# Optimization experiments

Measured on AMD Instinct MI355X. Metric: run time of the kernel, lower is better.

## Reference

```python
import jax, jax.numpy as jnp
import numpy as np

B, S, D = 4, 2048, 1024


def setup_inputs() -> dict:
    key = jax.random.key(0)
    k1, k2, k3, k4 = jax.random.split(key, 4)
    scale = 1.0 / np.sqrt(D)
    return {
        "X_emb": jax.random.normal(k1, (B, S, D), dtype=jnp.float32),
        "W_q": jax.random.normal(k2, (D, D), dtype=jnp.float32) * scale,
        "W_k": jax.random.normal(k3, (D, D), dtype=jnp.float32) * scale,
        "W_v": jax.random.normal(k4, (D, D), dtype=jnp.float32) * scale,
    }


def reference(X_emb, W_q, W_k, W_v):
    # nn.Linear(bias=False): x @ W.T
    Xq = jnp.einsum('bsd,ed->bse', X_emb, W_q)
    Xk = jnp.einsum('bsd,ed->bse', X_emb, W_k)
    Xv = jnp.einsum('bsd,ed->bse', X_emb, W_v)
    S_len = X_emb.shape[-2]
    # scores [B, S, S]; causal mask (strict upper triangle -> -inf)
    att = jnp.einsum('bqe,bke->bqk', Xq, Xk)
    causal = jnp.tril(jnp.ones((S_len, S_len), dtype=bool))
    att = jnp.where(causal, att, -jnp.inf)
    # note: original masks before scaling; -inf / sqrt(d) is still -inf
    att = att / jnp.sqrt(jnp.asarray(Xk.shape[-1], att.dtype))
    w = jax.nn.softmax(att, axis=-1)
    return jnp.einsum('bqk,bke->bqe', w, Xv)
```

## Files before the change

### kernel.cpp

```cpp
#include <hip/hip_runtime.h>
#include <stdint.h>
#include <math.h>

typedef __attribute__((ext_vector_type(8))) __bf16 bf16x8;
typedef __attribute__((ext_vector_type(4))) float f32x4;

__device__ __forceinline__ unsigned short f2bf(float f) {
    unsigned u = __float_as_uint(f);
    u += 0x7FFF + ((u >> 16) & 1);
    return (unsigned short)(u >> 16);
}
__device__ __forceinline__ float bf2f(unsigned short u) {
    return __uint_as_float((unsigned)u << 16);
}

__global__ __launch_bounds__(256)
void convt_k(const float* __restrict__ X, const float* __restrict__ Wq,
             const float* __restrict__ Wk, const float* __restrict__ Wv,
             unsigned short* __restrict__ Xb, unsigned short* __restrict__ WqT,
             unsigned short* __restrict__ WkT, unsigned short* __restrict__ Wvb,
             float* __restrict__ outz) {
    const int S = 2048, D = 1024;
    const int z = blockIdx.z;
    const int t = threadIdx.x;
    if (z == 7) {
        int gid = (blockIdx.y * 16 + blockIdx.x) * 256 + t;
        int stride = 512 * 256;
        float4 zz = (float4){0.f, 0.f, 0.f, 0.f};
        for (int i = gid; i < 4 * S * D / 4; i += stride)
            reinterpret_cast<float4*>(outz)[i] = zz;
        return;
    }
    const float* src;
    unsigned short* dstP = nullptr;
    unsigned short* dstT = nullptr;
    int rows;
    if (z < 4)      { src = X + (size_t)z * S * D; dstP = Xb + (size_t)z * S * D; rows = S; }
    else if (z == 4){ src = Wq; dstT = WqT; rows = D; }
    else if (z == 5){ src = Wk; dstT = WkT; rows = D; }
    else            { src = Wv; dstP = Wvb; rows = D; }
    const int r0 = blockIdx.y * 64, c0 = blockIdx.x * 64;
    if (r0 >= rows) return;

    __shared__ float tile[64][65];
    const int tr = t >> 4;
    const int tc4 = t & 15;
#pragma unroll
    for (int p = 0; p < 4; ++p) {
        int r = p * 16 + tr;
        float4 v = *reinterpret_cast<const float4*>(&src[(size_t)(r0 + r) * 1024 + c0 + tc4 * 4]);
        if (dstP) {
            ushort4 o; o.x = f2bf(v.x); o.y = f2bf(v.y); o.z = f2bf(v.z); o.w = f2bf(v.w);
            *reinterpret_cast<ushort4*>(&dstP[(size_t)(r0 + r) * 1024 + c0 + tc4 * 4]) = o;
        }
        if (dstT) {
            tile[r][tc4 * 4 + 0] = v.x; tile[r][tc4 * 4 + 1] = v.y;
            tile[r][tc4 * 4 + 2] = v.z; tile[r][tc4 * 4 + 3] = v.w;
        }
    }
    if (!dstT) return;
    __syncthreads();
#pragma unroll
    for (int p = 0; p < 4; ++p) {
        int c = p * 16 + tr;
        ushort4 o;
        o.x = f2bf(tile[tc4 * 4 + 0][c]);
        o.y = f2bf(tile[tc4 * 4 + 1][c]);
        o.z = f2bf(tile[tc4 * 4 + 2][c]);
        o.w = f2bf(tile[tc4 * 4 + 3][c]);
        *reinterpret_cast<ushort4*>(&dstT[(size_t)(c0 + c) * 1024 + r0 + tc4 * 4]) = o;
    }
}

__global__ __launch_bounds__(256)
void reduce4_k(const float* __restrict__ p, unsigned short* __restrict__ o, int n4) {
    const int slab = 1024 * 1024 / 4;
    int i = blockIdx.x * blockDim.x + threadIdx.x;
    int stride = gridDim.x * blockDim.x;
    for (; i < n4; i += stride) {
        float4 a = reinterpret_cast<const float4*>(p)[i];
        float4 b = reinterpret_cast<const float4*>(p)[i + slab];
        float4 c = reinterpret_cast<const float4*>(p)[i + 2 * slab];
        float4 d = reinterpret_cast<const float4*>(p)[i + 3 * slab];
        ushort4 u;
        u.x = f2bf(a.x + b.x + c.x + d.x);
        u.y = f2bf(a.y + b.y + c.y + d.y);
        u.z = f2bf(a.z + b.z + c.z + d.z);
        u.w = f2bf(a.w + b.w + c.w + d.w);
        reinterpret_cast<ushort4*>(o)[i] = u;
    }
}

__device__ __forceinline__ void gload16(const unsigned short* g, unsigned short* l) {
    __builtin_amdgcn_global_load_lds(
        (const __attribute__((address_space(1))) unsigned int*)g,
        (__attribute__((address_space(3))) unsigned int*)l, 16, 0, 0);
}

template <typename CT, bool ATOMIC>
__device__ __forceinline__ void core_tile(
    const unsigned short* __restrict__ A, const unsigned short* __restrict__ B,
    CT* __restrict__ C, int lda, int ldb, int ldc,
    int m0, int n0, int kst, int nk, float scale, bool first,
    unsigned short* AsB, unsigned short* BsB)
{
    const int t    = threadIdx.x;
    const int lane = t & 63;
    const int wid  = t >> 6;
    const int wm   = wid >> 1, wn = wid & 1;
    const int rsel = lane & 15;
    const int gsel = lane >> 4;
    const int srow = t >> 3;
    const int swz  = ((t & 7) ^ (srow & 7)) * 8;

    f32x4 acc[4][4];
#pragma unroll
    for (int m = 0; m < 4; ++m)
#pragma unroll
        for (int n = 0; n < 4; ++n) acc[m][n] = (f32x4){0.f, 0.f, 0.f, 0.f};

    const unsigned short* gpA[4];
    const unsigned short* gpB[4];
#pragma unroll
    for (int i = 0; i < 4; ++i) {
        gpA[i] = A + (long long)(m0 + srow + 32 * i) * lda + kst * 64 + swz;
        gpB[i] = B + (long long)(n0 + srow + 32 * i) * ldb + kst * 64 + swz;
    }

    auto stage = [&](int buf) {
#pragma unroll
        for (int i = 0; i < 4; ++i)
            gload16(gpA[i], &AsB[buf * 8192 + i * 2048 + t * 8]);
#pragma unroll
        for (int i = 0; i < 4; ++i)
            gload16(gpB[i], &BsB[buf * 8192 + i * 2048 + t * 8]);
#pragma unroll
        for (int i = 0; i < 4; ++i) { gpA[i] += 64; gpB[i] += 64; }
    };

    if (!first) {
        __builtin_amdgcn_s_barrier();
        __builtin_amdgcn_sched_barrier(0);
    }
    stage(0);

    for (int kt = 0; kt < nk; ++kt) {
        const int c = kt & 1;
        __builtin_amdgcn_s_barrier();
        __builtin_amdgcn_sched_barrier(0);
        if (kt + 1 < nk) {
            stage(c ^ 1);
            asm volatile("s_waitcnt vmcnt(8)" ::: "memory");
        } else {
            asm volatile("s_waitcnt vmcnt(0)" ::: "memory");
        }
        __builtin_amdgcn_s_barrier();
        __builtin_amdgcn_sched_barrier(0);

        bf16x8 aF[4][2], bF[4][2];
#pragma unroll
        for (int m = 0; m < 4; ++m)
#pragma unroll
            for (int ks = 0; ks < 2; ++ks) {
                int r  = wm * 64 + m * 16 + rsel;
                int cc = ks * 4 + gsel;
                aF[m][ks] = *reinterpret_cast<const bf16x8*>(
                    &AsB[c * 8192 + r * 64 + ((cc ^ (r & 7)) * 8)]);
            }
#pragma unroll
        for (int n = 0; n < 4; ++n)
#pragma unroll
            for (int ks = 0; ks < 2; ++ks) {
                int rb = wn * 64 + n * 16 + rsel;
                int cc = ks * 4 + gsel;
                bF[n][ks] = *reinterpret_cast<const bf16x8*>(
                    &BsB[c * 8192 + rb * 64 + ((cc ^ (rb & 7)) * 8)]);
            }

        __builtin_amdgcn_s_setprio(1);
#pragma unroll
        for (int m = 0; m < 4; ++m)
#pragma unroll
            for (int n = 0; n < 4; ++n)
#pragma unroll
                for (int ks = 0; ks < 2; ++ks)
                    acc[m][n] = __builtin_amdgcn_mfma_f32_16x16x32_bf16(
                        aF[m][ks], bF[n][ks], acc[m][n], 0, 0, 0);
        __builtin_amdgcn_s_setprio(0);
    }

    const int rowl = gsel * 4;
#pragma unroll
    for (int m = 0; m < 4; ++m)
#pragma unroll
        for (int n = 0; n < 4; ++n)
#pragma unroll
            for (int i = 0; i < 4; ++i) {
                int r  = m0 + wm * 64 + m * 16 + rowl + i;
                int cI = n0 + wn * 64 + n * 16 + rsel;
                float v = acc[m][n][i] * scale;
                if constexpr (sizeof(CT) == 2)
                    ((unsigned short*)C)[(long long)r * ldc + cI] = f2bf(v);
                else if constexpr (ATOMIC)
                    unsafeAtomicAdd((float*)&C[(long long)r * ldc + cI], v);
                else
                    ((float*)C)[(long long)r * ldc + cI] = v;
            }
}

__device__ __forceinline__ void tri_decode(int w, int& br, int& bc) {
    int rr = (int)((sqrtf(8.0f * (float)w + 1.0f) - 1.0f) * 0.5f);
    while ((rr + 1) * (rr + 2) / 2 <= w) ++rr;
    while (rr * (rr + 1) / 2 > w) --rr;
    br = rr; bc = w - rr * (rr + 1) / 2;
}

template <typename CT>
__global__ __launch_bounds__(256, 2)
void gemm0(const unsigned short* __restrict__ A, const unsigned short* __restrict__ B,
           CT* __restrict__ C, int lda, int ldb, int ldc, int K,
           long long sA, long long sB, long long sC, float scale)
{
    __shared__ unsigned short As[2 * 8192];
    __shared__ unsigned short Bs[2 * 8192];
    const int nbx = gridDim.x;
    const int nwg = nbx * gridDim.y;
    const int orig = blockIdx.y * nbx + blockIdx.x;
    const int q8 = nwg >> 3, r8 = nwg & 7;
    const int xcd = orig & 7, idx = orig >> 3;
    const int work = (xcd < r8 ? xcd * (q8 + 1) : r8 * (q8 + 1) + (xcd - r8) * q8) + idx;
    core_tile<CT, false>(A + (long long)blockIdx.z * sA, B + (long long)blockIdx.z * sB,
                         C + (long long)blockIdx.z * sC, lda, ldb, ldc,
                         (work / nbx) * 128, (work % nbx) * 128, 0, K >> 6, scale, true,
                         As, Bs);
}

__global__ __launch_bounds__(256, 2)
void gemm_xmvt(const unsigned short* __restrict__ Xb, const unsigned short* __restrict__ MTb,
               unsigned short* __restrict__ XMb, const unsigned short* __restrict__ Wv,
               unsigned short* __restrict__ Vt)
{
    const int S = 2048, D = 1024;
    const long long SD = (long long)S * D, DS = (long long)D * S;
    __shared__ unsigned short As[2 * 8192];
    __shared__ unsigned short Bs[2 * 8192];
    const int orig = blockIdx.x;
    const int work = (orig & 7) * 128 + (orig >> 3);
    if (work < 512) {
        int rw = work >> 3, c = work & 7;
        core_tile<unsigned short, false>(Xb, MTb, XMb, D, D, D,
            rw * 128, c * 128, 0, 16, 1.0f, true, As, Bs);
    } else {
        int v = work - 512;
        int b = v >> 7, u = v & 127;
        int r = u >> 4, c = u & 15;
        core_tile<unsigned short, false>(Wv, Xb + b * SD, Vt + b * DS, D, D, S,
            r * 128, c * 128, 0, 16, 1.0f, true, As, Bs);
    }
}

__global__ __launch_bounds__(256, 2)
void gemm_sc(const unsigned short* __restrict__ XM, const unsigned short* __restrict__ Xb,
             unsigned short* __restrict__ Sc)
{
    const int S = 2048, D = 1024;
    const long long SD = (long long)S * D, SS = (long long)S * S;
    __shared__ unsigned short As[2 * 8192];
    __shared__ unsigned short Bs[2 * 8192];
    const int orig = blockIdx.x;
    const int work = (orig & 7) * 68 + (orig >> 3);
    int b = work / 136, tt = work % 136;
    int br, bc;
    tri_decode(tt, br, bc);
    core_tile<unsigned short, false>(XM + b * SD, Xb + b * SD, Sc + b * SS,
        D, D, S, br * 128, bc * 128, 0, 16, 0.03125f, true, As, Bs);
}

__global__ __launch_bounds__(256, 2)
void gemm_pv(const unsigned short* __restrict__ P, const unsigned short* __restrict__ Vt,
             float* __restrict__ out)
{
    const int S = 2048, D = 1024;
    const long long SS = (long long)S * S, DS = (long long)D * S, SD = (long long)S * D;
    __shared__ unsigned short As[2 * 8192];
    __shared__ unsigned short Bs[2 * 8192];
    const int cnt[16]  = {64,32,64,64,32,64,64,32,64,64,32,64,32,32,32,32};
    const int rowt[16] = {15, 7,14,13, 6,12,11, 5,10, 9, 4, 8, 3, 2, 1, 0};
    const int isB[16]  = { 1, 0, 1, 1, 0, 1, 1, 0, 1, 1, 0, 1, 0, 0, 0, 0};
    int w = blockIdx.x, k = 0;
    while (w >= cnt[k]) { w -= cnt[k]; ++k; }
    const int r = rowt[k];
    if (isB[k]) {
        int b = w >> 4, u = w & 15, c = u >> 1, h = u & 1;
        core_tile<float, true>(P + b * SS, Vt + b * DS, out + b * SD, S, S, D,
            r * 128, c * 128, h * (r + 1), r + 1, 1.0f, true, As, Bs);
    } else {
        int b = w >> 3, c = w & 7;
        core_tile<float, false>(P + b * SS, Vt + b * DS, out + b * SD, S, S, D,
            r * 128, c * 128, 0, 2 * (r + 1), 1.0f, true, As, Bs);
    }
}

__device__ __forceinline__ float waveMax(float v) {
#pragma unroll
    for (int o = 32; o > 0; o >>= 1) v = fmaxf(v, __shfl_xor(v, o, 64));
    return v;
}
__device__ __forceinline__ float waveSum(float v) {
#pragma unroll
    for (int o = 32; o > 0; o >>= 1) v += __shfl_xor(v, o, 64);
    return v;
}

__global__ __launch_bounds__(256)
void softmax_causal(const unsigned short* __restrict__ S, unsigned short* __restrict__ P,
                    int Slen) {
    __shared__ float e[2048];
    __shared__ float red[4];
    long long row = blockIdx.x;
    int q = (int)(row % Slen);
    const unsigned short* srow = S + row * (long long)Slen;
    unsigned short* prow = P + row * (long long)Slen;
    int len = q + 1;
    int t = threadIdx.x;

    int n8 = len >> 3;
    float mx = -3.0e38f;
    for (int i = t; i < n8; i += 256) {
        uint4 v = reinterpret_cast<const uint4*>(srow)[i];
        float f0 = __uint_as_float(v.x << 16), f1 = __uint_as_float(v.x & 0xffff0000u);
        float f2 = __uint_as_float(v.y << 16), f3 = __uint_as_float(v.y & 0xffff0000u);
        float f4 = __uint_as_float(v.z << 16), f5 = __uint_as_float(v.z & 0xffff0000u);
        float f6 = __uint_as_float(v.w << 16), f7 = __uint_as_float(v.w & 0xffff0000u);
        e[8 * i + 0] = f0; e[8 * i + 1] = f1; e[8 * i + 2] = f2; e[8 * i + 3] = f3;
        e[8 * i + 4] = f4; e[8 * i + 5] = f5; e[8 * i + 6] = f6; e[8 * i + 7] = f7;
        mx = fmaxf(mx, fmaxf(fmaxf(fmaxf(f0, f1), fmaxf(f2, f3)),
                             fmaxf(fmaxf(f4, f5), fmaxf(f6, f7))));
    }
    if (t < (len & 7)) {
        float v = bf2f(srow[n8 * 8 + t]);
        e[n8 * 8 + t] = v;
        mx = fmaxf(mx, v);
    }
    mx = waveMax(mx);
    if ((t & 63) == 0) red[t >> 6] = mx;
    __syncthreads();
    mx = fmaxf(fmaxf(red[0], red[1]), fmaxf(red[2], red[3]));

    float sum = 0.f;
    for (int k = t; k < len; k += 256) {
        float v = __expf(e[k] - mx);
        e[k] = v;
        sum += v;
    }
    sum = waveSum(sum);
    __syncthreads();
    if ((t & 63) == 0) red[t >> 6] = sum;
    __syncthreads();
    sum = red[0] + red[1] + red[2] + red[3];
    float inv = 1.0f / sum;

    int wlim = ((q >> 7) + 1) << 7;
    __syncthreads();
    for (int i = t; i < (wlim >> 2); i += 256) {
        int k = 4 * i;
        ushort4 o;
        o.x = (k + 0 < len) ? f2bf(e[k + 0] * inv) : (unsigned short)0;
        o.y = (k + 1 < len) ? f2bf(e[k + 1] * inv) : (unsigned short)0;
        o.z = (k + 2 < len) ? f2bf(e[k + 2] * inv) : (unsigned short)0;
        o.w = (k + 3 < len) ? f2bf(e[k + 3] * inv) : (unsigned short)0;
        reinterpret_cast<ushort4*>(prow)[i] = o;
    }
}

extern "C" void kernel_launch(void* const* d_in, const int* in_sizes, int n_in,
                              void* d_out, int out_size, void* d_ws, size_t ws_size,
                              hipStream_t stream) {
    const int B = 4, S = 2048, D = 1024;
    const float* X  = (const float*)d_in[0];
    const float* Wq = (const float*)d_in[1];
    const float* Wk = (const float*)d_in[2];
    const float* Wv = (const float*)d_in[3];
    float* out = (float*)d_out;

    char* ws = (char*)d_ws;
    unsigned short* Xb    = (unsigned short*)ws; ws += (size_t)B * S * D * 2;
    unsigned short* WqT   = (unsigned short*)ws; ws += (size_t)D * D * 2;
    unsigned short* WkT   = (unsigned short*)ws; ws += (size_t)D * D * 2;
    unsigned short* Wvb   = (unsigned short*)ws; ws += (size_t)D * D * 2;
    unsigned short* MTb   = (unsigned short*)ws; ws += (size_t)D * D * 2;
    unsigned short* XMb   = (unsigned short*)ws; ws += (size_t)B * S * D * 2;
    unsigned short* Vt    = (unsigned short*)ws; ws += (size_t)B * D * S * 2;
    unsigned short* Sc    = (unsigned short*)ws; ws += (size_t)B * S * S * 2;
    unsigned short* P     = (unsigned short*)ws; ws += (size_t)B * S * S * 2;
    float*          Mpart = (float*)ws;          ws += (size_t)4 * D * D * 4;

    convt_k<<<dim3(16, 32, 8), 256, 0, stream>>>(X, Wq, Wk, Wv, Xb, WqT, WkT, Wvb, out);

    dim3 blk(256);
    gemm0<float><<<dim3(8, 8, 4), blk, 0, stream>>>(
        WkT, WqT, Mpart, D, D, D, 256, 256, 256, (long long)D * D, 1.0f);
    reduce4_k<<<1024, 256, 0, stream>>>(Mpart, MTb, D * D / 4);

    gemm_xmvt<<<dim3(1024, 1, 1), blk, 0, stream>>>(Xb, MTb, XMb, Wvb, Vt);

    gemm_sc<<<dim3(544, 1, 1), blk, 0, stream>>>(XMb, Xb, Sc);

    softmax_causal<<<B * S, 256, 0, stream>>>(Sc, P, S);

    gemm_pv<<<dim3(768, 1, 1), blk, 0, stream>>>(P, Vt, out);
}
```

Before: 169.0 us.

## Balance causal PV GEMM by pairing short and long row tiles per block

Replaces the table-driven PV work assignment, which split long rows into two atomic halves, with a pairing scheme. One block handles a short row tile together with part of the mirrored long row tile (15-r), and another block finishes the rest of that long row. The grid drops from 768 to 512 blocks with equal K-work per block, and blocks are swizzled across XCDs. The cost is more atomic accumulation on long-row outputs, and the launch must match the new decode exactly.

```diff
diff --git a/kernel.cpp b/kernel.cpp
--- a/kernel.cpp
+++ b/kernel.cpp
@@ -284,20 +284,27 @@
     const long long SS = (long long)S * S, DS = (long long)D * S, SD = (long long)S * D;
     __shared__ unsigned short As[2 * 8192];
     __shared__ unsigned short Bs[2 * 8192];
-    const int cnt[16]  = {64,32,64,64,32,64,64,32,64,64,32,64,32,32,32,32};
-    const int rowt[16] = {15, 7,14,13, 6,12,11, 5,10, 9, 4, 8, 3, 2, 1, 0};
-    const int isB[16]  = { 1, 0, 1, 1, 0, 1, 1, 0, 1, 1, 0, 1, 0, 0, 0, 0};
-    int w = blockIdx.x, k = 0;
-    while (w >= cnt[k]) { w -= cnt[k]; ++k; }
-    const int r = rowt[k];
-    if (isB[k]) {
-        int b = w >> 4, u = w & 15, c = u >> 1, h = u & 1;
-        core_tile<float, true>(P + b * SS, Vt + b * DS, out + b * SD, S, S, D,
-            r * 128, c * 128, h * (r + 1), r + 1, 1.0f, true, As, Bs);
+    const int orig = blockIdx.x;
+    const int work = (orig & 7) * 64 + (orig >> 3);
+    const int b = work >> 7;
+    const int u = work & 127;
+    const int r = u >> 4;
+    const int c = (u >> 1) & 7;
+    const int h = u & 1;
+    const unsigned short* Pb = P + b * SS;
+    const unsigned short* Vb = Vt + b * DS;
+    float* Ob = out + b * SD;
+    const int rb = 15 - r;
+    const int split = 15 - 2 * r;
+
+    if (h == 0) {
+        core_tile<float, false>(Pb, Vb, Ob, S, S, D,
+            r * 128, c * 128, 0, 2 * (r + 1), 1.0f, true, As, Bs);
+        core_tile<float, true>(Pb, Vb, Ob, S, S, D,
+            rb * 128, c * 128, 0, split, 1.0f, false, As, Bs);
     } else {
-        int b = w >> 3, c = w & 7;
-        core_tile<float, false>(P + b * SS, Vt + b * DS, out + b * SD, S, S, D,
-            r * 128, c * 128, 0, 2 * (r + 1), 1.0f, true, As, Bs);
+        core_tile<float, true>(Pb, Vb, Ob, S, S, D,
+            rb * 128, c * 128, split, 17, 1.0f, true, As, Bs);
     }
 }
 
@@ -408,5 +415,5 @@
 
     softmax_causal<<<B * S, 256, 0, stream>>>(Sc, P, S);
 
-    gemm_pv<<<dim3(768, 1, 1), blk, 0, stream>>>(P, Vt, out);
-}
+    gemm_pv<<<dim3(512, 1, 1), blk, 0, stream>>>(P, Vt, out);
+}
```

Result: faster. 164.7 us (-2.5%).

## Use 64-row tiles for causal score and PV GEMMs, drop split-K atomics

Applied to the files above, without the earlier changes.

Makes the GEMM core tile's M dimension a template parameter and uses 64x128 tiles for the causal score GEMM and the P·V GEMM. The finer row granularity follows the causal triangle more closely, so less masked work is computed. P·V no longer splits K with atomic adds, so zero-initialising the output in the conversion kernel is removed. Each block now has lower arithmetic intensity and there are more blocks to schedule, and long P·V rows run as single tiles without split-K balancing.

```diff
diff --git a/kernel.cpp b/kernel.cpp
--- a/kernel.cpp
+++ b/kernel.cpp
@@ -18,19 +18,10 @@
 void convt_k(const float* __restrict__ X, const float* __restrict__ Wq,
              const float* __restrict__ Wk, const float* __restrict__ Wv,
              unsigned short* __restrict__ Xb, unsigned short* __restrict__ WqT,
-             unsigned short* __restrict__ WkT, unsigned short* __restrict__ Wvb,
-             float* __restrict__ outz) {
+             unsigned short* __restrict__ WkT, unsigned short* __restrict__ Wvb) {
     const int S = 2048, D = 1024;
     const int z = blockIdx.z;
     const int t = threadIdx.x;
-    if (z == 7) {
-        int gid = (blockIdx.y * 16 + blockIdx.x) * 256 + t;
-        int stride = 512 * 256;
-        float4 zz = (float4){0.f, 0.f, 0.f, 0.f};
-        for (int i = gid; i < 4 * S * D / 4; i += stride)
-            reinterpret_cast<float4*>(outz)[i] = zz;
-        return;
-    }
     const float* src;
     unsigned short* dstP = nullptr;
     unsigned short* dstT = nullptr;
@@ -97,13 +88,14 @@
         (__attribute__((address_space(3))) unsigned int*)l, 16, 0, 0);
 }
 
-template <typename CT, bool ATOMIC>
+template <int FM, typename CT>
 __device__ __forceinline__ void core_tile(
     const unsigned short* __restrict__ A, const unsigned short* __restrict__ B,
     CT* __restrict__ C, int lda, int ldb, int ldc,
     int m0, int n0, int kst, int nk, float scale, bool first,
     unsigned short* AsB, unsigned short* BsB)
 {
+    constexpr int FN = 4;
     const int t    = threadIdx.x;
     const int lane = t & 63;
     const int wid  = t >> 6;
@@ -113,29 +105,32 @@
     const int srow = t >> 3;
     const int swz  = ((t & 7) ^ (srow & 7)) * 8;
 
-    f32x4 acc[4][4];
-#pragma unroll
-    for (int m = 0; m < 4; ++m)
-#pragma unroll
-        for (int n = 0; n < 4; ++n) acc[m][n] = (f32x4){0.f, 0.f, 0.f, 0.f};
-
-    const unsigned short* gpA[4];
+    f32x4 acc[FM][FN];
+#pragma unroll
+    for (int m = 0; m < FM; ++m)
+#pragma unroll
+        for (int n = 0; n < FN; ++n) acc[m][n] = (f32x4){0.f, 0.f, 0.f, 0.f};
+
+    const unsigned short* gpA[FM];
     const unsigned short* gpB[4];
 #pragma unroll
-    for (int i = 0; i < 4; ++i) {
+    for (int i = 0; i < FM; ++i)
         gpA[i] = A + (long long)(m0 + srow + 32 * i) * lda + kst * 64 + swz;
+#pragma unroll
+    for (int i = 0; i < 4; ++i)
         gpB[i] = B + (long long)(n0 + srow + 32 * i) * ldb + kst * 64 + swz;
-    }
 
     auto stage = [&](int buf) {
 #pragma unroll
-        for (int i = 0; i < 4; ++i)
-            gload16(gpA[i], &AsB[buf * 8192 + i * 2048 + t * 8]);
+        for (int i = 0; i < FM; ++i)
+            gload16(gpA[i], &AsB[buf * (FM * 2048) + i * 2048 + t * 8]);
 #pragma unroll
         for (int i = 0; i < 4; ++i)
             gload16(gpB[i], &BsB[buf * 8192 + i * 2048 + t * 8]);
 #pragma unroll
-        for (int i = 0; i < 4; ++i) { gpA[i] += 64; gpB[i] += 64; }
+        for (int i = 0; i < FM; ++i) gpA[i] += 64;
+#pragma unroll
+        for (int i = 0; i < 4; ++i) gpB[i] += 64;
     };
 
     if (!first) {
@@ -150,25 +145,26 @@
         __builtin_amdgcn_sched_barrier(0);
         if (kt + 1 < nk) {
             stage(c ^ 1);
-            asm volatile("s_waitcnt vmcnt(8)" ::: "memory");
+            if constexpr (FM == 4) asm volatile("s_waitcnt vmcnt(8)" ::: "memory");
+            else                   asm volatile("s_waitcnt vmcnt(6)" ::: "memory");
         } else {
             asm volatile("s_waitcnt vmcnt(0)" ::: "memory");
         }
         __builtin_amdgcn_s_barrier();
         __builtin_amdgcn_sched_barrier(0);
 
-        bf16x8 aF[4][2], bF[4][2];
-#pragma unroll
-        for (int m = 0; m < 4; ++m)
+        bf16x8 aF[FM][2], bF[FN][2];
+#pragma unroll
+        for (int m = 0; m < FM; ++m)
 #pragma unroll
             for (int ks = 0; ks < 2; ++ks) {
-                int r  = wm * 64 + m * 16 + rsel;
+                int r  = wm * (FM * 16) + m * 16 + rsel;
                 int cc = ks * 4 + gsel;
                 aF[m][ks] = *reinterpret_cast<const bf16x8*>(
-                    &AsB[c * 8192 + r * 64 + ((cc ^ (r & 7)) * 8)]);
+                    &AsB[c * (FM * 2048) + r * 64 + ((cc ^ (r & 7)) * 8)]);
             }
 #pragma unroll
-        for (int n = 0; n < 4; ++n)
+        for (int n = 0; n < FN; ++n)
 #pragma unroll
             for (int ks = 0; ks < 2; ++ks) {
                 int rb = wn * 64 + n * 16 + rsel;
@@ -179,9 +175,9 @@
 
         __builtin_amdgcn_s_setprio(1);
 #pragma unroll
-        for (int m = 0; m < 4; ++m)
-#pragma unroll
-            for (int n = 0; n < 4; ++n)
+        for (int m = 0; m < FM; ++m)
+#pragma unroll
+            for (int n = 0; n < FN; ++n)
 #pragma unroll
                 for (int ks = 0; ks < 2; ++ks)
                     acc[m][n] = __builtin_amdgcn_mfma_f32_16x16x32_bf16(
@@ -191,28 +187,19 @@
 
     const int rowl = gsel * 4;
 #pragma unroll
-    for (int m = 0; m < 4; ++m)
-#pragma unroll
-        for (int n = 0; n < 4; ++n)
+    for (int m = 0; m < FM; ++m)
+#pragma unroll
+        for (int n = 0; n < FN; ++n)
 #pragma unroll
             for (int i = 0; i < 4; ++i) {
-                int r  = m0 + wm * 64 + m * 16 + rowl + i;
+                int r  = m0 + wm * (FM * 16) + m * 16 + rowl + i;
                 int cI = n0 + wn * 64 + n * 16 + rsel;
                 float v = acc[m][n][i] * scale;
                 if constexpr (sizeof(CT) == 2)
                     ((unsigned short*)C)[(long long)r * ldc + cI] = f2bf(v);
-                else if constexpr (ATOMIC)
-                    unsafeAtomicAdd((float*)&C[(long long)r * ldc + cI], v);
                 else
                     ((float*)C)[(long long)r * ldc + cI] = v;
             }
-}
-
-__device__ __forceinline__ void tri_decode(int w, int& br, int& bc) {
-    int rr = (int)((sqrtf(8.0f * (float)w + 1.0f) - 1.0f) * 0.5f);
-    while ((rr + 1) * (rr + 2) / 2 <= w) ++rr;
-    while (rr * (rr + 1) / 2 > w) --rr;
-    br = rr; bc = w - rr * (rr + 1) / 2;
 }
 
 template <typename CT>
@@ -229,10 +216,10 @@
     const int q8 = nwg >> 3, r8 = nwg & 7;
     const int xcd = orig & 7, idx = orig >> 3;
     const int work = (xcd < r8 ? xcd * (q8 + 1) : r8 * (q8 + 1) + (xcd - r8) * q8) + idx;
-    core_tile<CT, false>(A + (long long)blockIdx.z * sA, B + (long long)blockIdx.z * sB,
-                         C + (long long)blockIdx.z * sC, lda, ldb, ldc,
-                         (work / nbx) * 128, (work % nbx) * 128, 0, K >> 6, scale, true,
-                         As, Bs);
+    core_tile<4, CT>(A + (long long)blockIdx.z * sA, B + (long long)blockIdx.z * sB,
+                     C + (long long)blockIdx.z * sC, lda, ldb, ldc,
+                     (work / nbx) * 128, (work % nbx) * 128, 0, K >> 6, scale, true,
+                     As, Bs);
 }
 
 __global__ __launch_bounds__(256, 2)
@@ -248,13 +235,13 @@
     const int work = (orig & 7) * 128 + (orig >> 3);
     if (work < 512) {
         int rw = work >> 3, c = work & 7;
-        core_tile<unsigned short, false>(Xb, MTb, XMb, D, D, D,
+        core_tile<4, unsigned short>(Xb, MTb, XMb, D, D, D,
             rw * 128, c * 128, 0, 16, 1.0f, true, As, Bs);
     } else {
         int v = work - 512;
         int b = v >> 7, u = v & 127;
         int r = u >> 4, c = u & 15;
-        core_tile<unsigned short, false>(Wv, Xb + b * SD, Vt + b * DS, D, D, S,
+        core_tile<4, unsigned short>(Wv, Xb + b * SD, Vt + b * DS, D, D, S,
             r * 128, c * 128, 0, 16, 1.0f, true, As, Bs);
     }
 }
@@ -265,15 +252,19 @@
 {
     const int S = 2048, D = 1024;
     const long long SD = (long long)S * D, SS = (long long)S * S;
-    __shared__ unsigned short As[2 * 8192];
+    __shared__ unsigned short As[2 * 4096];
     __shared__ unsigned short Bs[2 * 8192];
     const int orig = blockIdx.x;
-    const int work = (orig & 7) * 68 + (orig >> 3);
-    int b = work / 136, tt = work % 136;
-    int br, bc;
-    tri_decode(tt, br, bc);
-    core_tile<unsigned short, false>(XM + b * SD, Xb + b * SD, Sc + b * SS,
-        D, D, S, br * 128, bc * 128, 0, 16, 0.03125f, true, As, Bs);
+    const int work = (orig & 7) * 136 + (orig >> 3);
+    const int b = work / 272, j = work % 272;
+    int a = (int)((sqrtf(4.0f * (float)j + 1.0f) - 1.0f) * 0.5f);
+    while ((a + 1) * (a + 2) <= j) ++a;
+    while (a * (a + 1) > j) --a;
+    const int off = j - a * (a + 1);
+    const int r = 2 * a + (off > a ? 1 : 0);
+    const int c = (off > a) ? (off - a - 1) : off;
+    core_tile<2, unsigned short>(XM + b * SD, Xb + b * SD, Sc + b * SS,
+        D, D, S, r * 64, c * 128, 0, 16, 0.03125f, true, As, Bs);
 }
 
 __global__ __launch_bounds__(256, 2)
@@ -282,23 +273,14 @@
 {
     const int S = 2048, D = 1024;
     const long long SS = (long long)S * S, DS = (long long)D * S, SD = (long long)S * D;
-    __shared__ unsigned short As[2 * 8192];
+    __shared__ unsigned short As[2 * 4096];
     __shared__ unsigned short Bs[2 * 8192];
-    const int cnt[16]  = {64,32,64,64,32,64,64,32,64,64,32,64,32,32,32,32};
-    const int rowt[16] = {15, 7,14,13, 6,12,11, 5,10, 9, 4, 8, 3, 2, 1, 0};
-    const int isB[16]  = { 1, 0, 1, 1, 0, 1, 1, 0, 1, 1, 0, 1, 0, 0, 0, 0};
-    int w = blockIdx.x, k = 0;
-    while (w >= cnt[k]) { w -= cnt[k]; ++k; }
-    const int r = rowt[k];
-    if (isB[k]) {
-        int b = w >> 4, u = w & 15, c = u >> 1, h = u & 1;
-        core_tile<float, true>(P + b * SS, Vt + b * DS, out + b * SD, S, S, D,
-            r * 128, c * 128, h * (r + 1), r + 1, 1.0f, true, As, Bs);
-    } else {
-        int b = w >> 3, c = w & 7;
-        core_tile<float, false>(P + b * SS, Vt + b * DS, out + b * SD, S, S, D,
-            r * 128, c * 128, 0, 2 * (r + 1), 1.0f, true, As, Bs);
-    }
+    const int rank = blockIdx.x;
+    const int r = 31 - (rank >> 5);
+    const int u = rank & 31;
+    const int b = u >> 3, c = u & 7;
+    core_tile<2, float>(P + b * SS, Vt + b * DS, out + b * SD, S, S, D,
+        r * 64, c * 128, 0, r + 1, 1.0f, true, As, Bs);
 }
 
 __device__ __forceinline__ float waveMax(float v) {
@@ -395,7 +377,7 @@
     unsigned short* P     = (unsigned short*)ws; ws += (size_t)B * S * S * 2;
     float*          Mpart = (float*)ws;          ws += (size_t)4 * D * D * 4;
 
-    convt_k<<<dim3(16, 32, 8), 256, 0, stream>>>(X, Wq, Wk, Wv, Xb, WqT, WkT, Wvb, out);
+    convt_k<<<dim3(16, 32, 7), 256, 0, stream>>>(X, Wq, Wk, Wv, Xb, WqT, WkT, Wvb);
 
     dim3 blk(256);
     gemm0<float><<<dim3(8, 8, 4), blk, 0, stream>>>(
@@ -404,9 +386,9 @@
 
     gemm_xmvt<<<dim3(1024, 1, 1), blk, 0, stream>>>(Xb, MTb, XMb, Wvb, Vt);
 
-    gemm_sc<<<dim3(544, 1, 1), blk, 0, stream>>>(XMb, Xb, Sc);
+    gemm_sc<<<dim3(1088, 1, 1), blk, 0, stream>>>(XMb, Xb, Sc);
 
     softmax_causal<<<B * S, 256, 0, stream>>>(Sc, P, S);
 
-    gemm_pv<<<dim3(768, 1, 1), blk, 0, stream>>>(P, Vt, out);
-}
+    gemm_pv<<<dim3(1024, 1, 1), blk, 0, stream>>>(P, Vt, out);
+}
```

After: 145.4 us. -14.0%, faster.

## Split score GEMM along K into two buffers and rebalance PV split-K

Applied to the files above, without the earlier changes.

The score GEMM is split along the reduction dimension into two halves written to separate bf16 buffers, doubling the block count, and the softmax sums the two partials when it loads them. The PV GEMM replaces its fixed row table with a split-K scheme that gives each row tile 1 to 4 chunks according to its causal length, using atomic accumulation when there is more than one chunk. Zeroing of the output moves from the conversion kernel into softmax, and only for rows that need it. This aims to improve load balance and occupancy across CUs, at the cost of extra score traffic, more atomics and extra rounding from adding two bf16 partials.

```diff
diff --git a/kernel.cpp b/kernel.cpp
--- a/kernel.cpp
+++ b/kernel.cpp
@@ -18,19 +18,10 @@
 void convt_k(const float* __restrict__ X, const float* __restrict__ Wq,
              const float* __restrict__ Wk, const float* __restrict__ Wv,
              unsigned short* __restrict__ Xb, unsigned short* __restrict__ WqT,
-             unsigned short* __restrict__ WkT, unsigned short* __restrict__ Wvb,
-             float* __restrict__ outz) {
+             unsigned short* __restrict__ WkT, unsigned short* __restrict__ Wvb) {
     const int S = 2048, D = 1024;
     const int z = blockIdx.z;
     const int t = threadIdx.x;
-    if (z == 7) {
-        int gid = (blockIdx.y * 16 + blockIdx.x) * 256 + t;
-        int stride = 512 * 256;
-        float4 zz = (float4){0.f, 0.f, 0.f, 0.f};
-        for (int i = gid; i < 4 * S * D / 4; i += stride)
-            reinterpret_cast<float4*>(outz)[i] = zz;
-        return;
-    }
     const float* src;
     unsigned short* dstP = nullptr;
     unsigned short* dstT = nullptr;
@@ -261,19 +252,21 @@
 
 __global__ __launch_bounds__(256, 2)
 void gemm_sc(const unsigned short* __restrict__ XM, const unsigned short* __restrict__ Xb,
-             unsigned short* __restrict__ Sc)
+             unsigned short* __restrict__ ScA, unsigned short* __restrict__ ScB)
 {
     const int S = 2048, D = 1024;
     const long long SD = (long long)S * D, SS = (long long)S * S;
     __shared__ unsigned short As[2 * 8192];
     __shared__ unsigned short Bs[2 * 8192];
     const int orig = blockIdx.x;
-    const int work = (orig & 7) * 68 + (orig >> 3);
-    int b = work / 136, tt = work % 136;
+    const int work = (orig & 7) * 136 + (orig >> 3);
+    const int tile = work >> 1, half = work & 1;
+    const int b = tile / 136, tt = tile % 136;
     int br, bc;
     tri_decode(tt, br, bc);
-    core_tile<unsigned short, false>(XM + b * SD, Xb + b * SD, Sc + b * SS,
-        D, D, S, br * 128, bc * 128, 0, 16, 0.03125f, true, As, Bs);
+    unsigned short* dst = half ? ScB : ScA;
+    core_tile<unsigned short, false>(XM + b * SD, Xb + b * SD, dst + b * SS,
+        D, D, S, br * 128, bc * 128, half * 8, 8, 0.03125f, true, As, Bs);
 }
 
 __global__ __launch_bounds__(256, 2)
@@ -284,21 +277,27 @@
     const long long SS = (long long)S * S, DS = (long long)D * S, SD = (long long)S * D;
     __shared__ unsigned short As[2 * 8192];
     __shared__ unsigned short Bs[2 * 8192];
-    const int cnt[16]  = {64,32,64,64,32,64,64,32,64,64,32,64,32,32,32,32};
-    const int rowt[16] = {15, 7,14,13, 6,12,11, 5,10, 9, 4, 8, 3, 2, 1, 0};
-    const int isB[16]  = { 1, 0, 1, 1, 0, 1, 1, 0, 1, 1, 0, 1, 0, 0, 0, 0};
-    int w = blockIdx.x, k = 0;
-    while (w >= cnt[k]) { w -= cnt[k]; ++k; }
-    const int r = rowt[k];
-    if (isB[k]) {
-        int b = w >> 4, u = w & 15, c = u >> 1, h = u & 1;
+    const int orig = blockIdx.x;
+    const int work = (orig & 7) * 160 + (orig >> 3);
+    const int g = work / 40;
+    const int u = 39 - (work % 40);
+    const int b = g >> 3, c = g & 7;
+
+    int r, i, n;
+    if (u < 4)       { r = u;                 i = 0;           n = 1; }
+    else if (u < 12) { r = 4  + ((u - 4) >> 1);  i = (u - 4) & 1;  n = 2; }
+    else if (u < 24) { r = 8  + (u - 12) / 3;    i = (u - 12) % 3; n = 3; }
+    else             { r = 12 + ((u - 24) >> 2); i = (u - 24) & 3; n = 4; }
+    const int steps = 2 * (r + 1);
+    const int kst = i * steps / n;
+    const int nk  = (i + 1) * steps / n - kst;
+
+    if (n == 1)
+        core_tile<float, false>(P + b * SS, Vt + b * DS, out + b * SD, S, S, D,
+            r * 128, c * 128, kst, nk, 1.0f, true, As, Bs);
+    else
         core_tile<float, true>(P + b * SS, Vt + b * DS, out + b * SD, S, S, D,
-            r * 128, c * 128, h * (r + 1), r + 1, 1.0f, true, As, Bs);
-    } else {
-        int b = w >> 3, c = w & 7;
-        core_tile<float, false>(P + b * SS, Vt + b * DS, out + b * SD, S, S, D,
-            r * 128, c * 128, 0, 2 * (r + 1), 1.0f, true, As, Bs);
-    }
+            r * 128, c * 128, kst, nk, 1.0f, true, As, Bs);
 }
 
 __device__ __forceinline__ float waveMax(float v) {
@@ -313,32 +312,43 @@
 }
 
 __global__ __launch_bounds__(256)
-void softmax_causal(const unsigned short* __restrict__ S, unsigned short* __restrict__ P,
-                    int Slen) {
+void softmax_causal(const unsigned short* __restrict__ SA, const unsigned short* __restrict__ SB,
+                    unsigned short* __restrict__ P, float* __restrict__ out, int Slen) {
     __shared__ float e[2048];
     __shared__ float red[4];
     long long row = blockIdx.x;
     int q = (int)(row % Slen);
-    const unsigned short* srow = S + row * (long long)Slen;
+    const unsigned short* sa = SA + row * (long long)Slen;
+    const unsigned short* sb = SB + row * (long long)Slen;
     unsigned short* prow = P + row * (long long)Slen;
     int len = q + 1;
     int t = threadIdx.x;
 
+    if (q >= 512) {
+        float4 zz = (float4){0.f, 0.f, 0.f, 0.f};
+        reinterpret_cast<float4*>(out + row * 1024)[t] = zz;
+    }
+
     int n8 = len >> 3;
     float mx = -3.0e38f;
     for (int i = t; i < n8; i += 256) {
-        uint4 v = reinterpret_cast<const uint4*>(srow)[i];
-        float f0 = __uint_as_float(v.x << 16), f1 = __uint_as_float(v.x & 0xffff0000u);
-        float f2 = __uint_as_float(v.y << 16), f3 = __uint_as_float(v.y & 0xffff0000u);
-        float f4 = __uint_as_float(v.z << 16), f5 = __uint_as_float(v.z & 0xffff0000u);
-        float f6 = __uint_as_float(v.w << 16), f7 = __uint_as_float(v.w & 0xffff0000u);
+        uint4 va = reinterpret_cast<const uint4*>(sa)[i];
+        uint4 vb = reinterpret_cast<const uint4*>(sb)[i];
+        float f0 = __uint_as_float(va.x << 16) + __uint_as_float(vb.x << 16);
+        float f1 = __uint_as_float(va.x & 0xffff0000u) + __uint_as_float(vb.x & 0xffff0000u);
+        float f2 = __uint_as_float(va.y << 16) + __uint_as_float(vb.y << 16);
+        float f3 = __uint_as_float(va.y & 0xffff0000u) + __uint_as_float(vb.y & 0xffff0000u);
+        float f4 = __uint_as_float(va.z << 16) + __uint_as_float(vb.z << 16);
+        float f5 = __uint_as_float(va.z & 0xffff0000u) + __uint_as_float(vb.z & 0xffff0000u);
+        float f6 = __uint_as_float(va.w << 16) + __uint_as_float(vb.w << 16);
+        float f7 = __uint_as_float(va.w & 0xffff0000u) + __uint_as_float(vb.w & 0xffff0000u);
         e[8 * i + 0] = f0; e[8 * i + 1] = f1; e[8 * i + 2] = f2; e[8 * i + 3] = f3;
         e[8 * i + 4] = f4; e[8 * i + 5] = f5; e[8 * i + 6] = f6; e[8 * i + 7] = f7;
         mx = fmaxf(mx, fmaxf(fmaxf(fmaxf(f0, f1), fmaxf(f2, f3)),
                              fmaxf(fmaxf(f4, f5), fmaxf(f6, f7))));
     }
     if (t < (len & 7)) {
-        float v = bf2f(srow[n8 * 8 + t]);
+        float v = bf2f(sa[n8 * 8 + t]) + bf2f(sb[n8 * 8 + t]);
         e[n8 * 8 + t] = v;
         mx = fmaxf(mx, v);
     }
@@ -391,11 +401,12 @@
     unsigned short* MTb   = (unsigned short*)ws; ws += (size_t)D * D * 2;
     unsigned short* XMb   = (unsigned short*)ws; ws += (size_t)B * S * D * 2;
     unsigned short* Vt    = (unsigned short*)ws; ws += (size_t)B * D * S * 2;
-    unsigned short* Sc    = (unsigned short*)ws; ws += (size_t)B * S * S * 2;
+    unsigned short* ScA   = (unsigned short*)ws; ws += (size_t)B * S * S * 2;
+    unsigned short* ScB   = (unsigned short*)ws; ws += (size_t)B * S * S * 2;
     unsigned short* P     = (unsigned short*)ws; ws += (size_t)B * S * S * 2;
     float*          Mpart = (float*)ws;          ws += (size_t)4 * D * D * 4;
 
-    convt_k<<<dim3(16, 32, 8), 256, 0, stream>>>(X, Wq, Wk, Wv, Xb, WqT, WkT, Wvb, out);
+    convt_k<<<dim3(16, 32, 7), 256, 0, stream>>>(X, Wq, Wk, Wv, Xb, WqT, WkT, Wvb);
 
     dim3 blk(256);
     gemm0<float><<<dim3(8, 8, 4), blk, 0, stream>>>(
@@ -404,9 +415,9 @@
 
     gemm_xmvt<<<dim3(1024, 1, 1), blk, 0, stream>>>(Xb, MTb, XMb, Wvb, Vt);
 
-    gemm_sc<<<dim3(544, 1, 1), blk, 0, stream>>>(XMb, Xb, Sc);
-
-    softmax_causal<<<B * S, 256, 0, stream>>>(Sc, P, S);
-
-    gemm_pv<<<dim3(768, 1, 1), blk, 0, stream>>>(P, Vt, out);
-}
+    gemm_sc<<<dim3(1088, 1, 1), blk, 0, stream>>>(XMb, Xb, ScA, ScB);
+
+    softmax_causal<<<B * S, 256, 0, stream>>>(ScA, ScB, P, out, S);
+
+    gemm_pv<<<dim3(1280, 1, 1), blk, 0, stream>>>(P, Vt, out);
+}
```

Measured after the change: 183.0 us. +8.3%, slower.
